# Kernel optimization log

Measured on AMD Instinct MI355X. Metric: run time of the kernel, lower is better.

Reference implementation:

```python
import jax, jax.numpy as jnp
import numpy as np

B, S, D, H = 2, 2048, 1024, 16
DEPTH = D // H

def setup_inputs() -> dict:
    key = jax.random.key(0)
    ks = jax.random.split(key, 6)
    sc = 0.02
    return {
        "x": jax.random.normal(ks[0], (B, S, D), dtype=jnp.float32),
        "mask": jnp.ones((S, S), dtype=jnp.int32),
        "wq": jax.random.normal(ks[1], (D, D), dtype=jnp.float32) * sc,
        "bq": jnp.zeros((D,), dtype=jnp.float32),
        "wk": jax.random.normal(ks[2], (D, D), dtype=jnp.float32) * sc,
        "bk": jnp.zeros((D,), dtype=jnp.float32),
        "wv": jax.random.normal(ks[3], (D, D), dtype=jnp.float32) * sc,
        "bv": jnp.zeros((D,), dtype=jnp.float32),
        "wo": jax.random.normal(ks[4], (D, D), dtype=jnp.float32) * sc,
        "bo": jnp.zeros((D,), dtype=jnp.float32),
    }

def _split_heads(t):
    # [B,S,D] -> [B,H,S,depth]
    b, s, _ = t.shape
    return t.reshape(b, s, H, DEPTH).transpose(0, 2, 1, 3)

def reference(x, mask, wq, bq, wk, bk, wv, bv, wo, bo):
    q = _split_heads(x @ wq + bq)
    k = _split_heads(x @ wk + bk)
    v = _split_heads(x @ wv + bv)
    scale = 1.0 / jnp.sqrt(jnp.asarray(DEPTH, x.dtype))
    scores = jnp.einsum('bhqd,bhkd->bhqk', q, k) * scale
    # Faithful to original: band_part(ones,-1,0) is the LOWER triangle
    # (incl. diagonal), and it is ADDED times -1e9 -> lower triangle masked.
    s_len = mask.shape[0]
    tri = jnp.tril(jnp.ones((s_len, s_len), dtype=x.dtype))
    scores = scores + tri * (-1e9)
    attn = jax.nn.softmax(scores, axis=-1)  # dropout is identity at inference
    out = jnp.einsum('bhqk,bhkd->bhqd', attn, v)
    out = out.transpose(0, 2, 1, 3).reshape(x.shape[0], -1, D)
    return out @ wo + bo
```

## Files before the change

### kernel.cpp

```cpp
#include <hip/hip_runtime.h>
#include <hip/hip_bf16.h>


using bf16   = __bf16;
using bf16x2 = __attribute__((ext_vector_type(2))) __bf16;
using bf16x4 = __attribute__((ext_vector_type(4))) __bf16;
using bf16x8 = __attribute__((ext_vector_type(8))) __bf16;
using f32x4  = __attribute__((ext_vector_type(4))) float;
using uintx2 = __attribute__((ext_vector_type(2))) unsigned int;
using uintx4 = __attribute__((ext_vector_type(4))) unsigned int;

__device__ __forceinline__ void load_lds16(const void* g, void* l) {
  __builtin_amdgcn_global_load_lds(
      (const __attribute__((address_space(1))) void*)g,
      (__attribute__((address_space(3))) void*)l, 16, 0, 0);
}

__device__ __forceinline__ unsigned int packbf(float a, float b) {
  bf16x2 v;
  v[0] = (bf16)a;
  v[1] = (bf16)b;
  return __builtin_bit_cast(unsigned int, v);
}

__device__ __forceinline__ void xchg_p(unsigned int u, unsigned int v, int hi,
                                       unsigned int& f, unsigned int& s) {
#if __has_builtin(__builtin_amdgcn_permlane32_swap) && \
    __has_builtin(__builtin_amdgcn_permlane16_swap)
  uintx2 ab = __builtin_amdgcn_permlane32_swap(u, v, false, false);
  uintx2 fs = __builtin_amdgcn_permlane16_swap(ab[0], ab[1], false, false);
  f = fs[0];
  s = fs[1];
#else
  unsigned int a = (hi < 2) ? u : (unsigned int)__shfl_xor((int)v, 32);
  unsigned int b = (hi < 2) ? (unsigned int)__shfl_xor((int)u, 32) : v;
  unsigned int a16 = (unsigned int)__shfl_xor((int)a, 16);
  unsigned int b16 = (unsigned int)__shfl_xor((int)b, 16);
  f = (hi & 1) ? b16 : a;
  s = (hi & 1) ? b : a16;
#endif
}

__global__ __launch_bounds__(256) void prep_kernel(
    const float* __restrict__ x, bf16* __restrict__ xb,
    const float* __restrict__ wq, const float* __restrict__ wk,
    const float* __restrict__ wv, const float* __restrict__ wo,
    bf16* __restrict__ wT) {
  const int t = threadIdx.x;
  int bid = blockIdx.x;
  if (bid < 4096) {
    const int i = (bid * 256 + t) * 4;
    const float4 v = *(const float4*)(x + i);
    bf16x4 o;
    o[0] = (bf16)v.x; o[1] = (bf16)v.y; o[2] = (bf16)v.z; o[3] = (bf16)v.w;
    *(bf16x4*)(xb + i) = o;
    return;
  }
  bid -= 4096;
  const int sel = bid >> 8;
  const float* w = (sel == 0) ? wq : (sel == 1) ? wk : (sel == 2) ? wv : wo;
  bf16* out = wT + (size_t)sel * 1048576;
  __shared__ float tile[64][65];
  const int n0 = (bid & 15) * 64;
  const int k0 = ((bid >> 4) & 15) * 64;
#pragma unroll
  for (int p = 0; p < 4; ++p) {
    const int row = p * 16 + (t >> 4);
    const int c4  = (t & 15) * 4;
    const float4 v = *(const float4*)&w[(size_t)(k0 + row) * 1024 + n0 + c4];
    tile[row][c4 + 0] = v.x; tile[row][c4 + 1] = v.y;
    tile[row][c4 + 2] = v.z; tile[row][c4 + 3] = v.w;
  }
  __syncthreads();
#pragma unroll
  for (int p = 0; p < 4; ++p) {
    const int rn = p * 16 + (t >> 4);
    const int c4 = (t & 15) * 4;
    bf16x4 o;
#pragma unroll
    for (int j = 0; j < 4; ++j) o[j] = (bf16)tile[c4 + j][rn];
    *(bf16x4*)&out[(size_t)(n0 + rn) * 1024 + k0 + c4] = o;
  }
}

template <int MODE>
__global__ __launch_bounds__(256, 2) void gemm_bt(
    const bf16* __restrict__ A, const bf16* __restrict__ Bt,
    const float* __restrict__ bias0, const float* __restrict__ bias1,
    const float* __restrict__ bias2, bf16* __restrict__ qf,
    bf16* __restrict__ kf, bf16* __restrict__ vt, float* __restrict__ fout,
    int Nblocks) {
  __shared__ __align__(16) char smem[32768];
  char* sA = smem;
  char* sB = smem + 16384;
  const int tid = threadIdx.x;
  const int lane = tid & 63;
  const int w = tid >> 6;
  const int wm = w >> 1, wn = w & 1;
  const int bid = blockIdx.x;
  const int m0 = (bid / Nblocks) * 128;
  const int n0 = (bid % Nblocks) * 128;

  const char* Ab = (const char*)A;
  const char* Bb = (const char*)Bt;
  size_t srcA[4], srcB[4];
#pragma unroll
  for (int it = 0; it < 4; ++it) {
    const int o = it * 4096 + tid * 16;
    const int r = o >> 7;
    const int cg = ((o >> 4) & 7) ^ (r & 7);
    srcA[it] = (size_t)(m0 + r) * 2048 + cg * 16;
    srcB[it] = (size_t)(n0 + r) * 2048 + cg * 16;
  }

  f32x4 acc[4][4] = {};

  for (int kt = 0; kt < 16; ++kt) {
    const size_t kb = (size_t)kt * 128;
#pragma unroll
    for (int it = 0; it < 4; ++it) {
      load_lds16(Ab + srcA[it] + kb, sA + it * 4096 + w * 1024);
      load_lds16(Bb + srcB[it] + kb, sB + it * 4096 + w * 1024);
    }
    asm volatile("s_waitcnt vmcnt(0)" ::: "memory");
    __syncthreads();
#pragma unroll
    for (int ks = 0; ks < 2; ++ks) {
      bf16x8 aF[4], bF[4];
      const int g = (lane >> 4) + 4 * ks;
#pragma unroll
      for (int i = 0; i < 4; ++i) {
        const int ra = wm * 64 + i * 16 + (lane & 15);
        aF[i] = *(const bf16x8*)(sA + ra * 128 + ((g ^ (ra & 7)) << 4));
        const int rb = wn * 64 + i * 16 + (lane & 15);
        bF[i] = *(const bf16x8*)(sB + rb * 128 + ((g ^ (rb & 7)) << 4));
      }
#pragma unroll
      for (int mi = 0; mi < 4; ++mi)
#pragma unroll
        for (int ni = 0; ni < 4; ++ni)
          acc[mi][ni] = __builtin_amdgcn_mfma_f32_16x16x32_bf16(
              aF[mi], bF[ni], acc[mi][ni], 0, 0, 0);
    }
    __syncthreads();
  }

  const int cn = lane & 15;
  const int gq = lane >> 4;
#pragma unroll
  for (int mi = 0; mi < 4; ++mi) {
#pragma unroll
    for (int ni = 0; ni < 4; ++ni) {
      const int n  = n0 + wn * 64 + ni * 16 + cn;
      const int mb = m0 + wm * 64 + mi * 16 + 4 * gq;
      const f32x4 v = acc[mi][ni];
      if (MODE == 0) {
        const float bias =
            (n < 1024) ? bias0[n] : ((n < 2048) ? bias1[n - 1024] : bias2[n - 2048]);
        if (n < 2048) {
          bf16* dst = (n < 1024) ? qf : kf;
          const int nn = n & 1023;
#pragma unroll
          for (int j = 0; j < 4; ++j)
            dst[(size_t)(mb + j) * 1024 + nn] = (bf16)(v[j] + bias);
        } else {
          const int nn = n - 2048;
          const int hh = nn >> 6, dd = nn & 63;
          const int bb = mb >> 11, ss = mb & 2047;
          bf16x4 pk;
#pragma unroll
          for (int j = 0; j < 4; ++j) pk[j] = (bf16)(v[j] + bias);
          *(bf16x4*)(vt + ((size_t)((bb * 16 + hh) * 64 + dd) * 2048 + ss)) = pk;
        }
      } else {
        const float bias = bias0[n];
#pragma unroll
        for (int j = 0; j < 4; ++j)
          fout[(size_t)(mb + j) * 1024 + n] = v[j] + bias;
      }
    }
  }
}

__global__ __launch_bounds__(256, 2) void attn_kernel(
    const bf16* __restrict__ qf, const bf16* __restrict__ kf,
    const bf16* __restrict__ vt, bf16* __restrict__ ao,
    bf16* __restrict__ o2buf, float* __restrict__ mlbuf) {
  __shared__ __align__(16) char smem[32768];

  const int tid  = threadIdx.x;
  const int lane = tid & 63;
  const int hi   = lane >> 4;
  const int qlo  = lane & 15;
  const int w    = tid >> 6;
  const int u  = blockIdx.x >> 5;
  const int bh = blockIdx.x & 31;
  const int b = bh >> 4, h = bh & 15;

  const char* kbase = (const char*)kf + ((size_t)b * 2048) * 2048 + h * 128;
  const char* vbase = (const char*)vt + (size_t)bh * 262144;
  const char* qbb   = (const char*)qf + ((size_t)b * 2048) * 2048 + h * 128;

  const int sr  = tid >> 3;
  const int scg = (tid & 7) ^ (sr & 7);

  bf16x8 onesB;
#pragma unroll
  for (int i = 0; i < 8; ++i) onesB[i] = (bf16)1.0f;

  int nseg, sjq[2], skb[2], ske[2], smode[2];
  if (u < 8) {
    nseg = 1;
    sjq[0] = u; skb[0] = 2 * u; ske[0] = 2 * u + 17; smode[0] = 1;
    sjq[1] = 0; skb[1] = 0; ske[1] = 0; smode[1] = 0;
  } else {
    const int j = u - 8;
    nseg = 2;
    sjq[0] = j;      skb[0] = 2 * j + 17; ske[0] = 32; smode[0] = 2;
    sjq[1] = 15 - j; skb[1] = 30 - 2 * j; ske[1] = 32; smode[1] = 0;
  }

  for (int seg = 0; seg < nseg; ++seg) {
    const int jq = sjq[seg], kbeg = skb[seg], kend = ske[seg];
    const int mode = smode[seg];

    const int q0 = jq * 128;
    const int qb = q0 + w * 32;

    bf16x8 qA[2][2];
#pragma unroll
    for (int nt = 0; nt < 2; ++nt) {
      const char* qrow = qbb + (size_t)(qb + 16 * nt + qlo) * 2048;
#pragma unroll
      for (int ks = 0; ks < 2; ++ks) {
        qA[nt][ks] = *(const bf16x8*)(qrow + ks * 64 + hi * 16);
#pragma unroll
        for (int i = 0; i < 8; ++i)
          qA[nt][ks][i] = (bf16)(0.125f * (float)qA[nt][ks][i]);
      }
    }

    float m[2] = {-1e30f, -1e30f};
    f32x4 lacc[2] = {};
    f32x4 O[2][4] = {};

    auto STAGE = [&](int kt, int bufi) {
      char* dK = smem + bufi * 8192 + w * 1024;
      char* dV = smem + 16384 + bufi * 8192 + w * 1024;
      const int kn = kt * 64;
#pragma unroll
      for (int p = 0; p < 2; ++p) {
        load_lds16(kbase + (size_t)(kn + sr + 32 * p) * 2048 + scg * 16,
                   dK + p * 4096);
        load_lds16(vbase + (size_t)(sr + 32 * p) * 4096 + (size_t)kn * 2 +
                       scg * 16,
                   dV + p * 4096);
      }
    };

    STAGE(kbeg, 0);
    __syncthreads();

    for (int kt = kbeg; kt < kend; ++kt) {
      const int cur = (kt - kbeg) & 1;

      if (kt + 1 < kend) STAGE(kt + 1, cur ^ 1);

      const char* bK = smem + cur * 8192;
      const char* bV = smem + 16384 + cur * 8192;

      f32x4 sc[2][4] = {};
#pragma unroll
      for (int ks = 0; ks < 2; ++ks) {
        const int gg = hi + 4 * ks;
#pragma unroll
        for (int t = 0; t < 4; ++t) {
          const int rk = t * 16 + qlo;
          const bf16x8 kF =
              *(const bf16x8*)(bK + rk * 128 + ((gg ^ (rk & 7)) << 4));
          sc[0][t] = __builtin_amdgcn_mfma_f32_16x16x32_bf16(kF, qA[0][ks],
                                                             sc[0][t], 0, 0, 0);
          sc[1][t] = __builtin_amdgcn_mfma_f32_16x16x32_bf16(kF, qA[1][ks],
                                                             sc[1][t], 0, 0, 0);
        }
      }

      if (kt * 64 < q0 + 128) {
        const int k0t = kt * 64;
#pragma unroll
        for (int nt = 0; nt < 2; ++nt)
#pragma unroll
          for (int t = 0; t < 4; ++t)
#pragma unroll
            for (int j = 0; j < 4; ++j) {
              const int kk = k0t + t * 16 + 4 * hi + j;
              const int qq = qb + 16 * nt + qlo;
              if (kk <= qq) sc[nt][t][j] = -1e30f;
            }
      }

      float tm[2];
#pragma unroll
      for (int nt = 0; nt < 2; ++nt) {
        float v = sc[nt][0][0];
#pragma unroll
        for (int t = 0; t < 4; ++t)
#pragma unroll
          for (int j = 0; j < 4; ++j) v = fmaxf(v, sc[nt][t][j]);
        v = fmaxf(v, __shfl_xor(v, 16));
        v = fmaxf(v, __shfl_xor(v, 32));
        tm[nt] = v;
      }

      const bool grew = (tm[0] - m[0] > 8.0f) || (tm[1] - m[1] > 8.0f);
      if (__any(grew)) {
#pragma unroll
        for (int nt = 0; nt < 2; ++nt) {
          const float mn = fmaxf(m[nt], tm[nt]);
          const float al = __expf(m[nt] - mn);
          m[nt] = mn;
#pragma unroll
          for (int j = 0; j < 4; ++j) {
            const float alj = __shfl(al, 4 * hi + j);
            lacc[nt][j] *= alj;
#pragma unroll
            for (int dt = 0; dt < 4; ++dt) O[nt][dt][j] *= alj;
          }
        }
      }

      bf16x8 pA[2][2];
#pragma unroll
      for (int nt = 0; nt < 2; ++nt) {
        unsigned int W[4][2];
#pragma unroll
        for (int t = 0; t < 4; ++t)
#pragma unroll
          for (int p = 0; p < 2; ++p)
            W[t][p] = packbf(__expf(sc[nt][t][2 * p] - m[nt]),
                             __expf(sc[nt][t][2 * p + 1] - m[nt]));
#pragma unroll
        for (int ks = 0; ks < 2; ++ks) {
          uintx4 w4;
#pragma unroll
          for (int p = 0; p < 2; ++p) {
            unsigned int f, s;
            xchg_p(W[2 * ks][p], W[2 * ks + 1][p], hi, f, s);
            w4[p] = f;
            w4[2 + p] = s;
          }
          pA[nt][ks] = __builtin_bit_cast(bf16x8, w4);
          lacc[nt] = __builtin_amdgcn_mfma_f32_16x16x32_bf16(pA[nt][ks], onesB,
                                                             lacc[nt], 0, 0, 0);
        }
      }

#pragma unroll
      for (int ks = 0; ks < 2; ++ks) {
        const int gg = hi + 4 * ks;
#pragma unroll
        for (int dt = 0; dt < 4; ++dt) {
          const int rv = dt * 16 + qlo;
          const bf16x8 vF =
              *(const bf16x8*)(bV + rv * 128 + ((gg ^ (rv & 7)) << 4));
          O[0][dt] = __builtin_amdgcn_mfma_f32_16x16x32_bf16(pA[0][ks], vF,
                                                             O[0][dt], 0, 0, 0);
          O[1][dt] = __builtin_amdgcn_mfma_f32_16x16x32_bf16(pA[1][ks], vF,
                                                             O[1][dt], 0, 0, 0);
        }
      }
      __syncthreads();
    }

    if (mode == 0) {
#pragma unroll
      for (int nt = 0; nt < 2; ++nt)
#pragma unroll
        for (int j = 0; j < 4; ++j) {
          const float linv = (lacc[nt][j] > 0.f) ? 1.f / lacc[nt][j] : 0.f;
          const int qg = qb + 16 * nt + 4 * hi + j;
#pragma unroll
          for (int dt = 0; dt < 4; ++dt)
            ao[(size_t)(b * 2048 + qg) * 1024 + h * 64 + dt * 16 + qlo] =
                (bf16)(O[nt][dt][j] * linv);
        }
    } else {
      const int qtbh = jq * 32 + bh;
      const int slot = mode - 1;
#pragma unroll
      for (int nt = 0; nt < 2; ++nt)
#pragma unroll
        for (int j = 0; j < 4; ++j) {
          const int r = w * 32 + 16 * nt + 4 * hi + j;
#pragma unroll
          for (int dt = 0; dt < 4; ++dt) {
            const bf16 vv = (bf16)O[nt][dt][j];
            if (mode == 1)
              ao[(size_t)(b * 2048 + q0 + r) * 1024 + h * 64 + dt * 16 + qlo] =
                  vv;
            else
              o2buf[(size_t)(qtbh * 128 + r) * 64 + dt * 16 + qlo] = vv;
          }
        }
      if (qlo == 0) {
#pragma unroll
        for (int nt = 0; nt < 2; ++nt)
#pragma unroll
          for (int j = 0; j < 4; ++j)
            mlbuf[((qtbh * 2 + slot) * 2 + 1) * 128 +
                  (w * 32 + 16 * nt + 4 * hi + j)] = lacc[nt][j];
      }
      if (hi == 0) {
#pragma unroll
        for (int nt = 0; nt < 2; ++nt)
          mlbuf[((qtbh * 2 + slot) * 2 + 0) * 128 + (w * 32 + 16 * nt + qlo)] =
              m[nt];
      }
    }
    __syncthreads();
  }
}

__global__ __launch_bounds__(256) void combine_kernel(
    const bf16* __restrict__ o2buf, const float* __restrict__ mlbuf,
    bf16* __restrict__ ao) {
  const int qtbh = blockIdx.x;
  const int jq = qtbh >> 5, bh = qtbh & 31;
  const int b = bh >> 4, h = bh & 15;
  const int t = threadIdx.x;
  const int r = t >> 1;
  const int c0 = (t & 1) * 32;

  const float m1 = mlbuf[((qtbh * 2 + 0) * 2 + 0) * 128 + r];
  const float l1 = mlbuf[((qtbh * 2 + 0) * 2 + 1) * 128 + r];
  const float m2 = mlbuf[((qtbh * 2 + 1) * 2 + 0) * 128 + r];
  const float l2 = mlbuf[((qtbh * 2 + 1) * 2 + 1) * 128 + r];
  const float M  = fmaxf(m1, m2);
  const float w1 = __expf(m1 - M), w2 = __expf(m2 - M);
  const float denom = w1 * l1 + w2 * l2;
  const float linv = (denom > 0.f) ? 1.f / denom : 0.f;

  bf16* arow = ao + ((size_t)(b * 2048 + jq * 128 + r) * 1024 + h * 64 + c0);
  const bf16* o2row = o2buf + ((size_t)(qtbh * 128 + r) * 64 + c0);
#pragma unroll
  for (int i = 0; i < 4; ++i) {
    const bf16x8 o1 = *(const bf16x8*)(arow + i * 8);
    const bf16x8 o2 = *(const bf16x8*)(o2row + i * 8);
    bf16x8 o;
#pragma unroll
    for (int j = 0; j < 8; ++j)
      o[j] = (bf16)((w1 * (float)o1[j] + w2 * (float)o2[j]) * linv);
    *(bf16x8*)(arow + i * 8) = o;
  }
}

__global__ __launch_bounds__(256) void vmean_kernel(const bf16* __restrict__ vt,
                                                    bf16* __restrict__ ao) {
  const int tid = threadIdx.x;
  const int lane = tid & 63, w = tid >> 6;
  const int gw = blockIdx.x * 4 + w;
  const int bh = gw >> 6, d = gw & 63;
  const int b = bh >> 4, h = bh & 15;
  const bf16x8* p = (const bf16x8*)(vt + (size_t)gw * 2048 + lane * 32);
  float s = 0.f;
#pragma unroll
  for (int i = 0; i < 4; ++i) {
    const bf16x8 v = p[i];
#pragma unroll
    for (int j = 0; j < 8; ++j) s += (float)v[j];
  }
  for (int off = 1; off < 64; off <<= 1) s += __shfl_xor(s, off);
  if (lane == 0)
    ao[(size_t)(b * 2048 + 2047) * 1024 + h * 64 + d] = (bf16)(s * (1.f / 2048.f));
}

extern "C" void kernel_launch(void* const* d_in, const int* in_sizes, int n_in,
                              void* d_out, int out_size, void* d_ws,
                              size_t ws_size, hipStream_t stream) {
  const float* x  = (const float*)d_in[0];
  const float* wq = (const float*)d_in[2];
  const float* bq = (const float*)d_in[3];
  const float* wk = (const float*)d_in[4];
  const float* bk = (const float*)d_in[5];
  const float* wv = (const float*)d_in[6];
  const float* bv = (const float*)d_in[7];
  const float* wo = (const float*)d_in[8];
  const float* bo = (const float*)d_in[9];
  float* out = (float*)d_out;

  if (ws_size < (size_t)25165824 * 2) return;

  bf16* ws    = (bf16*)d_ws;
  bf16* xb    = ws;
  bf16* wqkvT = xb + 4194304;
  bf16* woT   = wqkvT + 3145728;
  bf16* qfp   = woT + 1048576;
  bf16* kfp   = qfp + 4194304;
  bf16* vtp   = kfp + 4194304;
  bf16* aop   = vtp + 4194304;

  bf16*  o2buf = xb;
  float* mlbuf = (float*)(xb + 2097152);

  prep_kernel<<<5120, 256, 0, stream>>>(x, xb, wq, wk, wv, wo, wqkvT);

  gemm_bt<0><<<32 * 24, 256, 0, stream>>>(xb, wqkvT, bq, bk, bv, qfp, kfp, vtp,
                                          nullptr, 24);
  attn_kernel<<<512, 256, 0, stream>>>(qfp, kfp, vtp, aop, o2buf, mlbuf);
  vmean_kernel<<<512, 256, 0, stream>>>(vtp, aop);
  combine_kernel<<<256, 256, 0, stream>>>(o2buf, mlbuf, aop);
  gemm_bt<1><<<32 * 8, 256, 0, stream>>>(aop, woT, bo, nullptr, nullptr, nullptr,
                                         nullptr, nullptr, out, 8);
}
```

Measured before the change: 108.0 us.

## Store K/V in MFMA fragment layout and load fragments directly from global

The QKV GEMM epilogue now writes K and V directly in a per-lane MFMA fragment-ordered layout. The attention kernel can then load each operand fragment with one 16-byte global load per lane, with no LDS staging, double buffering or barriers. The goal is to remove LDS traffic and block-wide synchronisation from the inner attention loop. In exchange, the kernel relies on the cache and global latency without explicit prefetch, and the GEMM epilogue writes K with scattered 2-byte stores. vmean is rewritten for the new V layout with fewer blocks.

```diff
diff --git a/kernel.cpp b/kernel.cpp
--- a/kernel.cpp
+++ b/kernel.cpp
@@ -88,7 +88,7 @@
     const bf16* __restrict__ A, const bf16* __restrict__ Bt,
     const float* __restrict__ bias0, const float* __restrict__ bias1,
     const float* __restrict__ bias2, bf16* __restrict__ qf,
-    bf16* __restrict__ kf, bf16* __restrict__ vt, float* __restrict__ fout,
+    bf16* __restrict__ kfr, bf16* __restrict__ vfr, float* __restrict__ fout,
     int Nblocks) {
   __shared__ __align__(16) char smem[32768];
   char* sA = smem;
@@ -157,20 +157,36 @@
       if (MODE == 0) {
         const float bias =
             (n < 1024) ? bias0[n] : ((n < 2048) ? bias1[n - 1024] : bias2[n - 2048]);
-        if (n < 2048) {
-          bf16* dst = (n < 1024) ? qf : kf;
-          const int nn = n & 1023;
+        if (n < 1024) {
 #pragma unroll
           for (int j = 0; j < 4; ++j)
-            dst[(size_t)(mb + j) * 1024 + nn] = (bf16)(v[j] + bias);
+            qf[(size_t)(mb + j) * 1024 + n] = (bf16)(v[j] + bias);
+        } else if (n < 2048) {
+          const int dg = n - 1024;
+          const int hh = dg >> 6, d = dg & 63;
+          const int ks = d >> 5, hl = (d >> 3) & 3, e = d & 7;
+          const int bb = mb >> 11, sl = mb & 2047;
+          const int ktt = sl >> 6, tt = (sl >> 4) & 3, ql = sl & 15;
+          bf16* dst = kfr +
+                      ((((size_t)(bb * 16 + hh) * 32 + ktt) * 4 + tt) * 2 + ks) *
+                          512 +
+                      (hl * 16 + ql) * 8 + e;
+#pragma unroll
+          for (int j = 0; j < 4; ++j) dst[j * 8] = (bf16)(v[j] + bias);
         } else {
-          const int nn = n - 2048;
-          const int hh = nn >> 6, dd = nn & 63;
-          const int bb = mb >> 11, ss = mb & 2047;
+          const int dg = n - 2048;
+          const int hh = dg >> 6, d = dg & 63;
+          const int dt = d >> 4, dc = d & 15;
+          const int bb = mb >> 11, sl = mb & 2047;
+          const int ktt = sl >> 6, ks = (sl >> 5) & 1, hl = (sl >> 3) & 3,
+                    e0 = sl & 7;
           bf16x4 pk;
 #pragma unroll
           for (int j = 0; j < 4; ++j) pk[j] = (bf16)(v[j] + bias);
-          *(bf16x4*)(vt + ((size_t)((bb * 16 + hh) * 64 + dd) * 2048 + ss)) = pk;
+          *(bf16x4*)(vfr +
+                     ((((size_t)(bb * 16 + hh) * 32 + ktt) * 4 + dt) * 2 + ks) *
+                         512 +
+                     (hl * 16 + dc) * 8 + e0) = pk;
         }
       } else {
         const float bias = bias0[n];
@@ -183,11 +199,9 @@
 }
 
 __global__ __launch_bounds__(256, 2) void attn_kernel(
-    const bf16* __restrict__ qf, const bf16* __restrict__ kf,
-    const bf16* __restrict__ vt, bf16* __restrict__ ao,
+    const bf16* __restrict__ qf, const bf16* __restrict__ kfr,
+    const bf16* __restrict__ vfr, bf16* __restrict__ ao,
     bf16* __restrict__ o2buf, float* __restrict__ mlbuf) {
-  __shared__ __align__(16) char smem[32768];
-
   const int tid  = threadIdx.x;
   const int lane = tid & 63;
   const int hi   = lane >> 4;
@@ -197,12 +211,9 @@
   const int bh = blockIdx.x & 31;
   const int b = bh >> 4, h = bh & 15;
 
-  const char* kbase = (const char*)kf + ((size_t)b * 2048) * 2048 + h * 128;
-  const char* vbase = (const char*)vt + (size_t)bh * 262144;
-  const char* qbb   = (const char*)qf + ((size_t)b * 2048) * 2048 + h * 128;
-
-  const int sr  = tid >> 3;
-  const int scg = (tid & 7) ^ (sr & 7);
+  const char* kfb = (const char*)kfr + (size_t)bh * 262144 + lane * 16;
+  const char* vfb = (const char*)vfr + (size_t)bh * 262144 + lane * 16;
+  const char* qbb = (const char*)qf + ((size_t)b * 2048) * 2048 + h * 128;
 
   bf16x8 onesB;
 #pragma unroll
@@ -244,46 +255,31 @@
     f32x4 lacc[2] = {};
     f32x4 O[2][4] = {};
 
-    auto STAGE = [&](int kt, int bufi) {
-      char* dK = smem + bufi * 8192 + w * 1024;
-      char* dV = smem + 16384 + bufi * 8192 + w * 1024;
-      const int kn = kt * 64;
-#pragma unroll
-      for (int p = 0; p < 2; ++p) {
-        load_lds16(kbase + (size_t)(kn + sr + 32 * p) * 2048 + scg * 16,
-                   dK + p * 4096);
-        load_lds16(vbase + (size_t)(sr + 32 * p) * 4096 + (size_t)kn * 2 +
-                       scg * 16,
-                   dV + p * 4096);
-      }
-    };
-
-    STAGE(kbeg, 0);
-    __syncthreads();
-
     for (int kt = kbeg; kt < kend; ++kt) {
-      const int cur = (kt - kbeg) & 1;
-
-      if (kt + 1 < kend) STAGE(kt + 1, cur ^ 1);
-
-      const char* bK = smem + cur * 8192;
-      const char* bV = smem + 16384 + cur * 8192;
+      const char* kT = kfb + (size_t)kt * 8192;
+      const char* vT = vfb + (size_t)kt * 8192;
+      bf16x8 kFr[2][4], vFr[2][4];
+#pragma unroll
+      for (int ks = 0; ks < 2; ++ks)
+#pragma unroll
+        for (int t = 0; t < 4; ++t)
+          kFr[ks][t] = *(const bf16x8*)(kT + (t * 2 + ks) * 1024);
+#pragma unroll
+      for (int ks = 0; ks < 2; ++ks)
+#pragma unroll
+        for (int dt = 0; dt < 4; ++dt)
+          vFr[ks][dt] = *(const bf16x8*)(vT + (dt * 2 + ks) * 1024);
 
       f32x4 sc[2][4] = {};
 #pragma unroll
-      for (int ks = 0; ks < 2; ++ks) {
-        const int gg = hi + 4 * ks;
+      for (int ks = 0; ks < 2; ++ks)
 #pragma unroll
         for (int t = 0; t < 4; ++t) {
-          const int rk = t * 16 + qlo;
-          const bf16x8 kF =
-              *(const bf16x8*)(bK + rk * 128 + ((gg ^ (rk & 7)) << 4));
-          sc[0][t] = __builtin_amdgcn_mfma_f32_16x16x32_bf16(kF, qA[0][ks],
-                                                             sc[0][t], 0, 0, 0);
-          sc[1][t] = __builtin_amdgcn_mfma_f32_16x16x32_bf16(kF, qA[1][ks],
-                                                             sc[1][t], 0, 0, 0);
-        }
-      }
+          sc[0][t] = __builtin_amdgcn_mfma_f32_16x16x32_bf16(
+              kFr[ks][t], qA[0][ks], sc[0][t], 0, 0, 0);
+          sc[1][t] = __builtin_amdgcn_mfma_f32_16x16x32_bf16(
+              kFr[ks][t], qA[1][ks], sc[1][t], 0, 0, 0);
+        }
 
       if (kt * 64 < q0 + 128) {
         const int k0t = kt * 64;
@@ -356,20 +352,14 @@
       }
 
 #pragma unroll
-      for (int ks = 0; ks < 2; ++ks) {
-        const int gg = hi + 4 * ks;
+      for (int ks = 0; ks < 2; ++ks)
 #pragma unroll
         for (int dt = 0; dt < 4; ++dt) {
-          const int rv = dt * 16 + qlo;
-          const bf16x8 vF =
-              *(const bf16x8*)(bV + rv * 128 + ((gg ^ (rv & 7)) << 4));
-          O[0][dt] = __builtin_amdgcn_mfma_f32_16x16x32_bf16(pA[0][ks], vF,
-                                                             O[0][dt], 0, 0, 0);
-          O[1][dt] = __builtin_amdgcn_mfma_f32_16x16x32_bf16(pA[1][ks], vF,
-                                                             O[1][dt], 0, 0, 0);
-        }
-      }
-      __syncthreads();
+          O[0][dt] = __builtin_amdgcn_mfma_f32_16x16x32_bf16(
+              pA[0][ks], vFr[ks][dt], O[0][dt], 0, 0, 0);
+          O[1][dt] = __builtin_amdgcn_mfma_f32_16x16x32_bf16(
+              pA[1][ks], vFr[ks][dt], O[1][dt], 0, 0, 0);
+        }
     }
 
     if (mode == 0) {
@@ -417,7 +407,6 @@
               m[nt];
       }
     }
-    __syncthreads();
   }
 }
 
@@ -454,24 +443,29 @@
   }
 }
 
-__global__ __launch_bounds__(256) void vmean_kernel(const bf16* __restrict__ vt,
+__global__ __launch_bounds__(256) void vmean_kernel(const bf16* __restrict__ vfr,
                                                     bf16* __restrict__ ao) {
   const int tid = threadIdx.x;
   const int lane = tid & 63, w = tid >> 6;
   const int gw = blockIdx.x * 4 + w;
-  const int bh = gw >> 6, d = gw & 63;
+  const int bh = gw >> 2, dt = gw & 3;
   const int b = bh >> 4, h = bh & 15;
-  const bf16x8* p = (const bf16x8*)(vt + (size_t)gw * 2048 + lane * 32);
+  const char* vfb = (const char*)vfr + (size_t)bh * 262144 + lane * 16;
   float s = 0.f;
-#pragma unroll
-  for (int i = 0; i < 4; ++i) {
-    const bf16x8 v = p[i];
-#pragma unroll
-    for (int j = 0; j < 8; ++j) s += (float)v[j];
-  }
-  for (int off = 1; off < 64; off <<= 1) s += __shfl_xor(s, off);
-  if (lane == 0)
-    ao[(size_t)(b * 2048 + 2047) * 1024 + h * 64 + d] = (bf16)(s * (1.f / 2048.f));
+  for (int kt = 0; kt < 32; ++kt) {
+#pragma unroll
+    for (int ks = 0; ks < 2; ++ks) {
+      const bf16x8 v =
+          *(const bf16x8*)(vfb + (size_t)kt * 8192 + (dt * 2 + ks) * 1024);
+#pragma unroll
+      for (int e = 0; e < 8; ++e) s += (float)v[e];
+    }
+  }
+  s += __shfl_xor(s, 16);
+  s += __shfl_xor(s, 32);
+  if ((lane >> 4) == 0)
+    ao[(size_t)(b * 2048 + 2047) * 1024 + h * 64 + dt * 16 + lane] =
+        (bf16)(s * (1.f / 2048.f));
 }
 
 extern "C" void kernel_launch(void* const* d_in, const int* in_sizes, int n_in,
@@ -495,19 +489,19 @@
   bf16* wqkvT = xb + 4194304;
   bf16* woT   = wqkvT + 3145728;
   bf16* qfp   = woT + 1048576;
-  bf16* kfp   = qfp + 4194304;
-  bf16* vtp   = kfp + 4194304;
-  bf16* aop   = vtp + 4194304;
+  bf16* kfrag = qfp + 4194304;
+  bf16* vfrag = kfrag + 4194304;
+  bf16* aop   = vfrag + 4194304;
 
   bf16*  o2buf = xb;
   float* mlbuf = (float*)(xb + 2097152);
 
   prep_kernel<<<5120, 256, 0, stream>>>(x, xb, wq, wk, wv, wo, wqkvT);
 
-  gemm_bt<0><<<32 * 24, 256, 0, stream>>>(xb, wqkvT, bq, bk, bv, qfp, kfp, vtp,
-                                          nullptr, 24);
-  attn_kernel<<<512, 256, 0, stream>>>(qfp, kfp, vtp, aop, o2buf, mlbuf);
-  vmean_kernel<<<512, 256, 0, stream>>>(vtp, aop);
+  gemm_bt<0><<<32 * 24, 256, 0, stream>>>(xb, wqkvT, bq, bk, bv, qfp, kfrag,
+                                          vfrag, nullptr, 24);
+  attn_kernel<<<512, 256, 0, stream>>>(qfp, kfrag, vfrag, aop, o2buf, mlbuf);
+  vmean_kernel<<<32, 256, 0, stream>>>(vfrag, aop);
   combine_kernel<<<256, 256, 0, stream>>>(o2buf, mlbuf, aop);
   gemm_bt<1><<<32 * 8, 256, 0, stream>>>(aop, woT, bo, nullptr, nullptr, nullptr,
                                          nullptr, nullptr, out, 8);
```

Result: no change. 106.0 us (-1.9%).
